# Kernel optimization log

Measured on AMD Instinct MI355X. Metric: run time of the kernel, lower is better.

The kernel has to match this reference:

```python
import jax, jax.numpy as jnp
import numpy as np

B, N_PER, F_IN, HID, DEG = 64, 1024, 64, 128, 16
N = B * N_PER
E = N * DEG

def _ceil_k(k):
    return -((-4 * k) // 5)  # ceil(0.8 * k), static python int

def setup_inputs():
    key = jax.random.key(0)
    ks = jax.random.split(key, 16)
    x = jax.random.normal(ks[0], (N, F_IN), jnp.float32)
    # edges are intra-graph: local endpoints in [0, N_PER) offset by graph id
    loc = jax.random.randint(ks[1], (2, E), 0, N_PER, jnp.int32)
    gid = jnp.repeat(jnp.arange(B, dtype=jnp.int32), E // B)
    edge_index = loc + gid[None, :] * N_PER
    batch = jnp.repeat(jnp.arange(B, dtype=jnp.int32), N_PER)
    def lin(k, fi, fo):
        s = 1.0 / float(np.sqrt(fi))
        return jax.random.uniform(k, (fi, fo), jnp.float32, -s, s)
    inp = dict(x=x, edge_index=edge_index, batch=batch)
    inp["Wr1"] = lin(ks[2], F_IN, HID); inp["Wn1"] = lin(ks[3], F_IN, HID); inp["b1"] = jnp.zeros((HID,), jnp.float32)
    inp["Wr2"] = lin(ks[4], HID, HID); inp["Wn2"] = lin(ks[5], HID, HID); inp["b2"] = jnp.zeros((HID,), jnp.float32)
    inp["Wr3"] = lin(ks[6], HID, HID); inp["Wn3"] = lin(ks[7], HID, HID); inp["b3"] = jnp.zeros((HID,), jnp.float32)
    inp["p1"] = jax.random.normal(ks[8], (HID,), jnp.float32)
    inp["p2"] = jax.random.normal(ks[9], (HID,), jnp.float32)
    inp["p3"] = jax.random.normal(ks[10], (HID,), jnp.float32)
    inp["l1w"] = lin(ks[11], 2 * HID, HID); inp["l1b"] = jnp.zeros((HID,), jnp.float32)
    inp["l2w"] = lin(ks[12], HID, 2); inp["l2b"] = jnp.zeros((2,), jnp.float32)
    return inp

def _graph_conv(x, src, dst, emask, Wr, Wn, b, n_nodes):
    # x'_i = W1 x_i + sum_{j->i} W2 x_j + b ; masked edges contribute 0
    msg = x[src] * emask[:, None]                                  # [E, H]
    agg = jax.ops.segment_sum(msg, dst, num_segments=n_nodes)     # [N, H]
    return x @ Wr + agg @ Wn + b

def _topk_pool(x, src, dst, emask, p, k_prev):
    # PyG TopKPooling: score = x.p/||p||, keep ceil(0.8*n) per graph,
    # x_out = x[perm] * tanh(score[perm]); relabel+filter edges
    k_new = _ceil_k(k_prev)
    s = (x @ p) / jnp.linalg.norm(p)                               # [B*k_prev]
    vals, idx = jax.lax.top_k(s.reshape(B, k_prev), k_new)        # [B, k_new]
    perm = (idx + jnp.arange(B, dtype=idx.dtype)[:, None] * k_prev).reshape(-1)
    x_new = x[perm] * jnp.tanh(vals.reshape(-1))[:, None]
    inv = jnp.full((B * k_prev,), -1, jnp.int32).at[perm].set(jnp.arange(B * k_new, dtype=jnp.int32))
    ns, nd = inv[src], inv[dst]
    valid = emask * ((ns >= 0) & (nd >= 0)).astype(x.dtype)
    return x_new, jnp.maximum(ns, 0), jnp.maximum(nd, 0), valid, k_new

def _readout(x, k):
    b = jnp.repeat(jnp.arange(B, dtype=jnp.int32), k)
    gmax = jax.ops.segment_max(x, b, num_segments=B)
    gmean = jax.ops.segment_sum(x, b, num_segments=B) / k
    return jnp.concatenate([gmax, gmean], axis=1)                  # [B, 2H]

def reference(x, edge_index, batch, Wr1, Wn1, b1, Wr2, Wn2, b2, Wr3, Wn3, b3, p1, p2, p3, l1w, l1b, l2w, l2b):
    src, dst = edge_index[0], edge_index[1]
    emask = jnp.ones((E,), x.dtype)
    k = N_PER
    convs = [(Wr1, Wn1, b1), (Wr2, Wn2, b2), (Wr3, Wn3, b3)]
    pools = [p1, p2, p3]
    xs = []
    for (Wr, Wn, bb), p in zip(convs, pools):
        x = jax.nn.relu(_graph_conv(x, src, dst, emask, Wr, Wn, bb, B * k))
        x, src, dst, emask, k = _topk_pool(x, src, dst, emask, p, k)
        xs.append(_readout(x, k))
    h = xs[0] + xs[1] + xs[2]
    h = jax.nn.relu(h @ l1w + l1b)
    # F.dropout(p=0.5) skipped: eval-mode reference
    h = jax.nn.relu(h @ l2w + l2b)
    return jax.nn.log_softmax(h, axis=-1)
```

## Files before the change

### kernel.cpp

```cpp
#include <hip/hip_runtime.h>
#include <hip/hip_bf16.h>
#include <math.h>

#define NN   65536
#define NPER 1024
#define NE   1048576
#define NB   64

typedef __attribute__((ext_vector_type(8))) short short8;
typedef __attribute__((ext_vector_type(4))) float f32x4;


__global__ __launch_bounds__(256) void count_kernel(const int* __restrict__ ei, int* __restrict__ cnt){
  int e = blockIdx.x*256 + threadIdx.x;
  if (e < NE) atomicAdd(&cnt[ei[NE + e]], 1);
}

__global__ __launch_bounds__(1024) void scan1_kernel(const int* __restrict__ cnt,
      int* __restrict__ loc, int* __restrict__ bsum){
  __shared__ int wsum[16];
  int t = threadIdx.x;
  int i = blockIdx.x*1024 + t;
  int lane = t & 63, wid = t >> 6;
  int v = cnt[i];
  int s = v;
  #pragma unroll
  for (int d = 1; d < 64; d <<= 1){
    int src = (lane >= d) ? (lane - d) : lane;
    int u = __shfl(s, src);
    if (lane >= d) s += u;
  }
  if (lane == 63) wsum[wid] = s;
  __syncthreads();
  if (wid == 0){
    int ws = (lane < 16) ? wsum[lane] : 0;
    #pragma unroll
    for (int d = 1; d < 16; d <<= 1){
      int src = (lane >= d) ? (lane - d) : lane;
      int u = __shfl(ws, src);
      if (lane >= d) ws += u;
    }
    if (lane < 16) wsum[lane] = ws;
  }
  __syncthreads();
  int base = (wid > 0) ? wsum[wid - 1] : 0;
  loc[i] = base + s - v;
  if (t == 1023) bsum[blockIdx.x] = base + s;
}

__global__ __launch_bounds__(64) void scan2_kernel(const int* __restrict__ bsum, int* __restrict__ boff){
  int t = threadIdx.x;
  int v = bsum[t];
  int s = v;
  #pragma unroll
  for (int d = 1; d < 64; d <<= 1){
    int src = (t >= d) ? (t - d) : t;
    int u = __shfl(s, src);
    if (t >= d) s += u;
  }
  boff[t] = s - v;
}

__global__ __launch_bounds__(1024) void scan3_kernel(const int* __restrict__ loc, const int* __restrict__ boff,
      int* __restrict__ off, int* __restrict__ cursor){
  int i = blockIdx.x*1024 + threadIdx.x;
  int v = loc[i] + boff[blockIdx.x];
  off[i] = v;
  cursor[i] = v;
  if (i == NN - 1) off[NN] = NE;
}

__global__ __launch_bounds__(256) void fill_kernel(const int* __restrict__ ei, int* cursor, int* __restrict__ adj){
  int e = blockIdx.x*256 + threadIdx.x;
  if (e < NE){
    int pos = atomicAdd(&cursor[ei[NE + e]], 1);
    adj[pos] = ei[e];
  }
}


__global__ __launch_bounds__(1024) void compact_kernel(const int* __restrict__ off, const int* __restrict__ adj,
      const float* __restrict__ scale, const int* __restrict__ alive,
      int* __restrict__ adj2, float* __restrict__ scl2, int* __restrict__ deg2){
  int w = blockIdx.x*16 + ((int)threadIdx.x >> 6);
  int lane = threadIdx.x & 63;
  if (!alive[w]){ if (lane == 0) deg2[w] = 0; return; }
  int s0 = off[w], s1 = off[w+1];
  int base = s0;
  for (int e0 = s0; e0 < s1; e0 += 64){
    int e = e0 + lane;
    bool okE = e < s1;
    int s = adj[okE ? e : (s1 - 1)];
    float t = scale[s];
    bool keep = okE && (t != 0.f);
    unsigned long long m = __ballot(keep);
    int pos = base + __popcll(m & ((1ull << lane) - 1ull));
    if (keep){ adj2[pos] = s << 9; scl2[pos] = t; }
    base += __popcll(m);
  }
  if (lane == 0) deg2[w] = base - s0;
}


__global__ __launch_bounds__(1024) void gather_kernel(const float* __restrict__ x, int F,
      const int* __restrict__ off, const int* __restrict__ adjB, const float* __restrict__ scl,
      const int* __restrict__ deg2, float* __restrict__ agg, const int* __restrict__ alive){
  int bid = blockIdx.x;
  bid = (bid & 7) * (gridDim.x >> 3) + (bid >> 3);
  int w = bid*16 + ((int)threadIdx.x >> 6);
  int lane = threadIdx.x & 63;
  if (alive && !alive[w]) return;
  int s0 = off[w];
  int s1 = deg2 ? (s0 + deg2[w]) : off[w+1];
  if (F == 64){
    const char* xb = (const char*)x + (lane & 15)*16;
    int sub = lane >> 4;
    float4 a0 = make_float4(0.f,0.f,0.f,0.f), a1 = a0;
    if (s1 > s0){
      for (int e = s0; e < s1; e += 8){
        int e0 = e + sub, e1 = e + 4 + sub;
        bool ok0 = e0 < s1, ok1 = e1 < s1;
        size_t oA = (size_t)(unsigned)adjB[ok0 ? e0 : (s1 - 1)] << 8;
        size_t oB = (size_t)(unsigned)adjB[ok1 ? e1 : (s1 - 1)] << 8;
        float t0 = ok0 ? 1.f : 0.f, t1 = ok1 ? 1.f : 0.f;
        float4 vA = *(const float4*)(xb + oA);
        float4 vB = *(const float4*)(xb + oB);
        a0.x = fmaf(vA.x, t0, a0.x); a0.y = fmaf(vA.y, t0, a0.y);
        a0.z = fmaf(vA.z, t0, a0.z); a0.w = fmaf(vA.w, t0, a0.w);
        a1.x = fmaf(vB.x, t1, a1.x); a1.y = fmaf(vB.y, t1, a1.y);
        a1.z = fmaf(vB.z, t1, a1.z); a1.w = fmaf(vB.w, t1, a1.w);
      }
    }
    a0.x += a1.x; a0.y += a1.y; a0.z += a1.z; a0.w += a1.w;
    #pragma unroll
    for (int m = 16; m <= 32; m <<= 1){
      a0.x += __shfl_xor(a0.x, m);
      a0.y += __shfl_xor(a0.y, m);
      a0.z += __shfl_xor(a0.z, m);
      a0.w += __shfl_xor(a0.w, m);
    }
    if (lane < 16) *(float4*)&agg[(size_t)w*128 + (lane & 15)*4] = a0;
  } else {
    const char* xb = (const char*)x + (lane & 31)*16;
    int sub = lane >> 5;
    float4 a[4];
    #pragma unroll
    for (int i = 0; i < 4; ++i) a[i] = make_float4(0.f,0.f,0.f,0.f);
    if (s1 > s0){
      for (int e = s0; e < s1; e += 8){
        int ss[4]; float tv[4];
        #pragma unroll
        for (int i = 0; i < 4; ++i){
          int ei = e + 2*i + sub;
          bool okE = ei < s1;
          int ii = okE ? ei : (s1 - 1);
          ss[i] = adjB[ii];
          tv[i] = okE ? scl[ii] : 0.f;
        }
        #pragma unroll
        for (int i = 0; i < 4; ++i){
          float4 v = *(const float4*)(xb + (size_t)(unsigned)ss[i]);
          a[i].x = fmaf(v.x, tv[i], a[i].x);
          a[i].y = fmaf(v.y, tv[i], a[i].y);
          a[i].z = fmaf(v.z, tv[i], a[i].z);
          a[i].w = fmaf(v.w, tv[i], a[i].w);
        }
      }
    }
    float4 r;
    r.x = (a[0].x + a[1].x) + (a[2].x + a[3].x);
    r.y = (a[0].y + a[1].y) + (a[2].y + a[3].y);
    r.z = (a[0].z + a[1].z) + (a[2].z + a[3].z);
    r.w = (a[0].w + a[1].w) + (a[2].w + a[3].w);
    r.x += __shfl_xor(r.x, 32);
    r.y += __shfl_xor(r.y, 32);
    r.z += __shfl_xor(r.z, 32);
    r.w += __shfl_xor(r.w, 32);
    if (lane < 32) *(float4*)&agg[(size_t)w*128 + (lane & 31)*4] = r;
  }
}


__global__ __launch_bounds__(256) void wsplit_all_kernel(
      const float* __restrict__ Wr0, const float* __restrict__ Wn0,
      const float* __restrict__ Wr1, const float* __restrict__ Wn1,
      const float* __restrict__ Wr2, const float* __restrict__ Wn2,
      unsigned short* __restrict__ WTh, unsigned short* __restrict__ WTl){
  int idx = blockIdx.x*256 + threadIdx.x;
  int rel, Kcat, Kx, base;
  const float *Wr, *Wn;
  if (idx < 16384){ rel = idx;          Kcat = 128; Kx = 64;  base = 0;     Wr = Wr0; Wn = Wn0; }
  else if (idx < 49152){ rel = idx - 16384; Kcat = 256; Kx = 128; base = 16384; Wr = Wr1; Wn = Wn1; }
  else { rel = idx - 49152; Kcat = 256; Kx = 128; base = 49152; Wr = Wr2; Wn = Wn2; }
  int c = rel & 127, k = rel >> 7;
  float w = (k < Kx) ? Wr[k*128 + c] : Wn[(k - Kx)*128 + c];
  __hip_bfloat16 h = __float2bfloat16(w);
  float hf = __bfloat162float(h);
  __hip_bfloat16 l = __float2bfloat16(w - hf);
  WTh[base + c*Kcat + k] = reinterpret_cast<unsigned short&>(h);
  WTl[base + c*Kcat + k] = reinterpret_cast<unsigned short&>(l);
}


__global__ __launch_bounds__(256, 2) void conv_kernel(const float* __restrict__ xsrc, int strideX, int ntx,
      const float* aggb, int nta,
      const unsigned short* __restrict__ WTh, const unsigned short* __restrict__ WTl, int Kcat,
      const float* __restrict__ bias, const float* __restrict__ p, const float* __restrict__ scaleX,
      float* yout, float* __restrict__ score){
  __shared__ unsigned short XhL[128*32], XlL[128*32];
  __shared__ unsigned short WhL[128*32], WlL[128*32];
  __shared__ float sbuf[128*2];
  const int tid = threadIdx.x;
  const int row0 = blockIdx.x * 128;
  const int srow = tid & 127;
  const int shalf = tid >> 7;
  const int lane = tid & 63;
  const int wid = tid >> 6;
  const int wr = wid >> 1, wc = wid & 1;
  const int l15 = lane & 15, lkq = lane >> 4;

  const float xscale = scaleX ? scaleX[row0 + srow] : 1.f;

  f32x4 acc[4][4];
  #pragma unroll
  for (int m = 0; m < 4; ++m)
    #pragma unroll
    for (int j = 0; j < 4; ++j)
      acc[m][j] = (f32x4){0.f, 0.f, 0.f, 0.f};

  const int nt = ntx + nta;
  for (int t = 0; t < nt; ++t){
    __syncthreads();
    {
      const float* Xs   = (t < ntx) ? xsrc : aggb;
      const int stride  = (t < ntx) ? strideX : 128;
      const int kc      = (t < ntx) ? t*32 : (t - ntx)*32;
      const float sc    = (t < ntx) ? xscale : 1.f;
      #pragma unroll
      for (int kq2 = 0; kq2 < 2; ++kq2){
        const int kq = shalf*2 + kq2;
        const float* xp = Xs + (size_t)(row0 + srow)*stride + kc + kq*8;
        float4 v0 = *(const float4*)(xp);
        float4 v1 = *(const float4*)(xp + 4);
        float vv[8] = {v0.x*sc, v0.y*sc, v0.z*sc, v0.w*sc,
                       v1.x*sc, v1.y*sc, v1.z*sc, v1.w*sc};
        short8 hs, ls;
        #pragma unroll
        for (int q = 0; q < 8; ++q){
          __hip_bfloat16 h = __float2bfloat16(vv[q]);
          float hf = __bfloat162float(h);
          __hip_bfloat16 lo = __float2bfloat16(vv[q] - hf);
          hs[q] = reinterpret_cast<short&>(h);
          ls[q] = reinterpret_cast<short&>(lo);
        }
        const int kqph = kq ^ (srow & 3);
        *(short8*)&XhL[srow*32 + kqph*8] = hs;
        *(short8*)&XlL[srow*32 + kqph*8] = ls;
      }
      const int kcw = t*32;
      #pragma unroll
      for (int kq2 = 0; kq2 < 2; ++kq2){
        const int kq = shalf*2 + kq2;
        short8 h = *(const short8*)&WTh[(size_t)srow*Kcat + kcw + kq*8];
        short8 l = *(const short8*)&WTl[(size_t)srow*Kcat + kcw + kq*8];
        const int kqph = kq ^ (srow & 3);
        *(short8*)&WhL[srow*32 + kqph*8] = h;
        *(short8*)&WlL[srow*32 + kqph*8] = l;
      }
    }
    __syncthreads();
    short8 bh[4], bl[4];
    #pragma unroll
    for (int j = 0; j < 4; ++j){
      const int col = wc*64 + j*16 + l15;
      const int offb = col*32 + (lkq ^ (col & 3))*8;
      bh[j] = *(const short8*)&WhL[offb];
      bl[j] = *(const short8*)&WlL[offb];
    }
    #pragma unroll
    for (int m = 0; m < 4; ++m){
      const int row = wr*64 + m*16 + l15;
      const int offa = row*32 + (lkq ^ (row & 3))*8;
      short8 ah = *(const short8*)&XhL[offa];
      short8 al = *(const short8*)&XlL[offa];
      #pragma unroll
      for (int j = 0; j < 4; ++j){
        acc[m][j] = __builtin_amdgcn_mfma_f32_16x16x32_bf16(ah, bh[j], acc[m][j], 0, 0, 0);
        acc[m][j] = __builtin_amdgcn_mfma_f32_16x16x32_bf16(ah, bl[j], acc[m][j], 0, 0, 0);
        acc[m][j] = __builtin_amdgcn_mfma_f32_16x16x32_bf16(al, bh[j], acc[m][j], 0, 0, 0);
      }
    }
  }

  #pragma unroll
  for (int m = 0; m < 4; ++m){
    float prt[4] = {0.f, 0.f, 0.f, 0.f};
    #pragma unroll
    for (int j = 0; j < 4; ++j){
      const int col = wc*64 + j*16 + l15;
      const float bcol = bias[col];
      const float pcol = p[col];
      f32x4 a = acc[m][j];
      #pragma unroll
      for (int r = 0; r < 4; ++r){
        const int row = wr*64 + m*16 + lkq*4 + r;
        float y = fmaxf(a[r] + bcol, 0.f);
        yout[(size_t)(row0 + row)*128 + col] = y;
        prt[r] = fmaf(y, pcol, prt[r]);
      }
    }
    #pragma unroll
    for (int r = 0; r < 4; ++r){
      #pragma unroll
      for (int msk = 8; msk >= 1; msk >>= 1) prt[r] += __shfl_xor(prt[r], msk);
      if (l15 == 0) sbuf[(wr*64 + m*16 + lkq*4 + r)*2 + wc] = prt[r];
    }
  }
  __syncthreads();
  if (tid < 128) score[row0 + tid] = sbuf[tid*2] + sbuf[tid*2 + 1];
}


__global__ __launch_bounds__(1024) void topk_kernel(const float* __restrict__ score, const int* __restrict__ alive_cur,
      int* __restrict__ alive_next, float* __restrict__ scale, const float* __restrict__ p, int m){
  __shared__ float lv[1024];
  __shared__ int   li[1024];
  __shared__ float rnorm;
  const int g = blockIdx.x, t = threadIdx.x;
  if (t < 64){
    float v0 = p[t], v1 = p[t + 64];
    float ss = v0*v0 + v1*v1;
    #pragma unroll
    for (int mm = 32; mm >= 1; mm >>= 1) ss += __shfl_xor(ss, mm);
    if (t == 0) rnorm = rsqrtf(ss);
  }
  const int node = g*NPER + t;
  bool ok = alive_cur ? (alive_cur[node] != 0) : true;
  float v = ok ? score[node] : -INFINITY;
  int idx = node;
  alive_next[node] = 0;
  scale[node] = 0.f;

  auto cex_shfl = [&](int stride, bool dirUp){
    float vj = __shfl_xor(v, stride);
    int   ij = __shfl_xor(idx, stride);
    bool iAmLow = (t & stride) == 0;
    bool mineFirst = (v > vj) || (v == vj && idx < ij);
    bool takeMine = ((dirUp == iAmLow) == mineFirst);
    v   = takeMine ? v   : vj;
    idx = takeMine ? idx : ij;
  };
  auto cex_lds = [&](int stride, bool dirUp){
    __syncthreads();
    lv[t] = v; li[t] = idx;
    __syncthreads();
    float vj = lv[t ^ stride];
    int   ij = li[t ^ stride];
    bool iAmLow = (t & stride) == 0;
    bool mineFirst = (v > vj) || (v == vj && idx < ij);
    bool takeMine = ((dirUp == iAmLow) == mineFirst);
    v   = takeMine ? v   : vj;
    idx = takeMine ? idx : ij;
  };

  #pragma unroll
  for (int size = 2; size <= 64; size <<= 1){
    const bool dirUp = (t & size) == 0;
    for (int stride = size >> 1; stride >= 1; stride >>= 1)
      cex_shfl(stride, dirUp);
  }
  #pragma unroll
  for (int size = 128; size <= 1024; size <<= 1){
    const bool dirUp = (t & size) == 0;
    for (int stride = size >> 1; stride >= 64; stride >>= 1)
      cex_lds(stride, dirUp);
    for (int stride = 32; stride >= 1; stride >>= 1)
      cex_shfl(stride, dirUp);
  }

  if (t < m){
    alive_next[idx] = 1;
    scale[idx] = tanhf(v * rnorm);
  }
}


__global__ __launch_bounds__(1024) void readout_kernel(const float* __restrict__ y,
      const int* __restrict__ alive, const float* __restrict__ scale,
      float* __restrict__ h, int m){
  __shared__ float smx[64][17];
  __shared__ float ssm[64][17];
  int g = blockIdx.x;
  int fq = blockIdx.y;
  int t = threadIdx.x;
  int c  = t >> 4;
  int lf = t & 15;
  int f  = fq*16 + lf;
  int base = g*NPER;
  float mx[4] = {-INFINITY, -INFINITY, -INFINITY, -INFINITY};
  float sm[4] = {0.f, 0.f, 0.f, 0.f};
  #pragma unroll
  for (int i = 0; i < 16; i += 4){
    #pragma unroll
    for (int q = 0; q < 4; ++q){
      int node = base + c + (i + q)*64;
      int al = alive[node];
      float o = y[(size_t)node*128 + f] * scale[node];
      mx[q] = al ? fmaxf(mx[q], o) : mx[q];
      sm[q] += o;
    }
  }
  float mxa = fmaxf(fmaxf(mx[0], mx[1]), fmaxf(mx[2], mx[3]));
  float sma = (sm[0] + sm[1]) + (sm[2] + sm[3]);
  smx[c][lf] = mxa; ssm[c][lf] = sma;
  __syncthreads();
  for (int s = 32; s > 0; s >>= 1){
    if (c < s){
      smx[c][lf] = fmaxf(smx[c][lf], smx[c+s][lf]);
      ssm[c][lf] += ssm[c+s][lf];
    }
    __syncthreads();
  }
  if (c == 0){
    h[g*256 + f]       += smx[0][lf];
    h[g*256 + 128 + f] += ssm[0][lf] / (float)m;
  }
}


__global__ __launch_bounds__(128) void final_kernel(const float* __restrict__ h,
      const float* __restrict__ l1w, const float* __restrict__ l1b,
      const float* __restrict__ l2w, const float* __restrict__ l2b,
      float* __restrict__ out){
  int g = blockIdx.x, t = threadIdx.x;
  __shared__ float hrow[256];
  __shared__ float red0[128], red1[128];
  hrow[t]       = h[g*256 + t];
  hrow[t + 128] = h[g*256 + 128 + t];
  __syncthreads();
  float a = l1b[t];
  for (int k = 0; k < 256; ++k) a = fmaf(hrow[k], l1w[k*128 + t], a);
  a = fmaxf(a, 0.f);
  red0[t] = a * l2w[t*2 + 0];
  red1[t] = a * l2w[t*2 + 1];
  __syncthreads();
  for (int s = 64; s > 0; s >>= 1){
    if (t < s){ red0[t] += red0[t + s]; red1[t] += red1[t + s]; }
    __syncthreads();
  }
  if (t == 0){
    float z0 = fmaxf(red0[0] + l2b[0], 0.f);
    float z1 = fmaxf(red1[0] + l2b[1], 0.f);
    float mz = fmaxf(z0, z1);
    float lse = mz + logf(expf(z0 - mz) + expf(z1 - mz));
    out[g*2 + 0] = z0 - lse;
    out[g*2 + 1] = z1 - lse;
  }
}


static inline size_t alignup(size_t x){ return (x + 255) & ~(size_t)255; }

extern "C" void kernel_launch(void* const* d_in, const int* in_sizes, int n_in,
                              void* d_out, int out_size, void* d_ws, size_t ws_size,
                              hipStream_t stream) {
  const float* x_in = (const float*)d_in[0];
  const int*   ei   = (const int*)d_in[1];
  const float* Wr[3] = {(const float*)d_in[3], (const float*)d_in[6], (const float*)d_in[9]};
  const float* Wn[3] = {(const float*)d_in[4], (const float*)d_in[7], (const float*)d_in[10]};
  const float* bs[3] = {(const float*)d_in[5], (const float*)d_in[8], (const float*)d_in[11]};
  const float* ps[3] = {(const float*)d_in[12], (const float*)d_in[13], (const float*)d_in[14]};
  const float* l1w = (const float*)d_in[15];
  const float* l1b = (const float*)d_in[16];
  const float* l2w = (const float*)d_in[17];
  const float* l2b = (const float*)d_in[18];
  float* out = (float*)d_out;

  char* w = (char*)d_ws;
  size_t o = 0;
  auto take = [&](size_t bytes) -> void* { void* p = w + o; o = alignup(o + bytes); return p; };
  int*   off    = (int*)  take((size_t)(NN + 1) * 4);
  int*   adj    = (int*)  take((size_t)NE * 4);
  int*   adj2   = (int*)  take((size_t)NE * 4);
  float* scl2   = (float*)take((size_t)NE * 4);
  int*   deg2   = (int*)  take((size_t)NN * 4);
  int*   cnt    = (int*)  take((size_t)NN * 4);
  int*   loc    = (int*)  take((size_t)NN * 4);
  int*   cursor = (int*)  take((size_t)NN * 4);
  int*   bsum   = (int*)  take(64 * 4);
  int*   boff   = (int*)  take(64 * 4);
  int*   aliveA = (int*)  take((size_t)NN * 4);
  int*   aliveB = (int*)  take((size_t)NN * 4);
  float* scale  = (float*)take((size_t)NN * 4);
  float* score  = (float*)take((size_t)NN * 4);
  float* h      = (float*)take((size_t)NB * 256 * 4);
  unsigned short* WTh = (unsigned short*)take((size_t)81920 * 2);
  unsigned short* WTl = (unsigned short*)take((size_t)81920 * 2);
  float* A      = (float*)take((size_t)NN * 128 * 4);
  float* Bb     = (float*)take((size_t)NN * 128 * 4);
  (void)ws_size; (void)n_in; (void)in_sizes; (void)out_size;

  hipMemsetAsync(cnt, 0, (size_t)NN * 4, stream);
  count_kernel<<<NE/256, 256, 0, stream>>>(ei, cnt);
  scan1_kernel<<<NN/1024, 1024, 0, stream>>>(cnt, loc, bsum);
  scan2_kernel<<<1, 64, 0, stream>>>(bsum, boff);
  scan3_kernel<<<NN/1024, 1024, 0, stream>>>(loc, boff, off, cursor);
  fill_kernel<<<NE/256, 256, 0, stream>>>(ei, cursor, adj);
  hipMemsetAsync(h, 0, (size_t)NB * 256 * 4, stream);
  wsplit_all_kernel<<<320, 256, 0, stream>>>(Wr[0], Wn[0], Wr[1], Wn[1], Wr[2], Wn[2], WTh, WTl);

  const int MS[3]   = {820, 656, 525};
  const int WOFF[3] = {0, 16384, 49152};
  const int KCAT[3] = {128, 256, 256};
  int* aliveCur = nullptr;
  int* aliveNext = aliveA;
  float* bufs[2] = {Bb, A};
  for (int l = 0; l < 3; ++l){
    const int Kx = (l == 0) ? 64 : 128;
    const int Ka = (l == 0) ? 64 : 128;
    float* aggb = bufs[l & 1];
    if (l == 0){
      gather_kernel<<<NN/16, 1024, 0, stream>>>(x_in, 64, off, adj, nullptr, nullptr, aggb, nullptr);
      conv_kernel<<<NN/128, 256, 0, stream>>>(x_in, 64, Kx/32, aggb, Ka/32, WTh + WOFF[0], WTl + WOFF[0], KCAT[0],
                                              bs[0], ps[0], nullptr, aggb, score);
    } else {
      const float* ysrc = bufs[(l - 1) & 1];
      compact_kernel<<<NN/16, 1024, 0, stream>>>(off, adj, scale, aliveCur, adj2, scl2, deg2);
      gather_kernel<<<NN/16, 1024, 0, stream>>>(ysrc, 128, off, adj2, scl2, deg2, aggb, aliveCur);
      conv_kernel<<<NN/128, 256, 0, stream>>>(ysrc, 128, Kx/32, aggb, Ka/32, WTh + WOFF[l], WTl + WOFF[l], KCAT[l],
                                              bs[l], ps[l], scale, aggb, score);
    }
    topk_kernel<<<NB, 1024, 0, stream>>>(score, aliveCur, aliveNext, scale, ps[l], MS[l]);
    readout_kernel<<<dim3(NB, 8), 1024, 0, stream>>>(aggb, aliveNext, scale, h, MS[l]);
    aliveCur = aliveNext;
    aliveNext = (l == 0) ? aliveB : aliveA;
  }
  final_kernel<<<NB, 128, 0, stream>>>(h, l1w, l1b, l2w, l2b, out);
}
```

Baseline: 325.8 us.

## Fuse CSR build per graph and merge topk, readout and compaction into one kernel

Builds the CSR in a single per-graph kernel that uses a shared-memory histogram, scan and fill. This replaces the count/scan/fill chain, its memsets and its global atomics, and it relies on edges being contiguous and intra-graph per block of EPG. It also merges topk, readout and edge compaction into one per-graph tail kernel that keeps scale and alive in shared memory, which removes several launches and global round trips. The cost is that the readout and compaction now run on only 64 blocks, one per graph, so parallelism drops sharply for those phases.

```diff
diff --git a/kernel.cpp b/kernel.cpp
--- a/kernel.cpp
+++ b/kernel.cpp
@@ -6,23 +6,31 @@
 #define NPER 1024
 #define NE   1048576
 #define NB   64
+#define EPG  16384
 
 typedef __attribute__((ext_vector_type(8))) short short8;
 typedef __attribute__((ext_vector_type(4))) float f32x4;
 
 
-__global__ __launch_bounds__(256) void count_kernel(const int* __restrict__ ei, int* __restrict__ cnt){
-  int e = blockIdx.x*256 + threadIdx.x;
-  if (e < NE) atomicAdd(&cnt[ei[NE + e]], 1);
-}
-
-__global__ __launch_bounds__(1024) void scan1_kernel(const int* __restrict__ cnt,
-      int* __restrict__ loc, int* __restrict__ bsum){
+__global__ __launch_bounds__(1024) void csr_kernel(const int* __restrict__ ei,
+      int* __restrict__ off, int* __restrict__ adj){
+  __shared__ int hist[1024];
   __shared__ int wsum[16];
-  int t = threadIdx.x;
-  int i = blockIdx.x*1024 + t;
+  const int g = blockIdx.x, t = threadIdx.x;
+  const int ebase = g*EPG, nbase = g*NPER;
+  hist[t] = 0;
+  __syncthreads();
+  int srcs[16], dls[16];
+  #pragma unroll
+  for (int i = 0; i < 16; ++i){
+    int e = ebase + t + i*1024;
+    srcs[i] = ei[e];
+    dls[i]  = ei[NE + e] - nbase;
+    atomicAdd(&hist[dls[i]], 1);
+  }
+  __syncthreads();
+  int v = hist[t];
   int lane = t & 63, wid = t >> 6;
-  int v = cnt[i];
   int s = v;
   #pragma unroll
   for (int d = 1; d < 64; d <<= 1){
@@ -44,61 +52,17 @@
   }
   __syncthreads();
   int base = (wid > 0) ? wsum[wid - 1] : 0;
-  loc[i] = base + s - v;
-  if (t == 1023) bsum[blockIdx.x] = base + s;
-}
-
-__global__ __launch_bounds__(64) void scan2_kernel(const int* __restrict__ bsum, int* __restrict__ boff){
-  int t = threadIdx.x;
-  int v = bsum[t];
-  int s = v;
-  #pragma unroll
-  for (int d = 1; d < 64; d <<= 1){
-    int src = (t >= d) ? (t - d) : t;
-    int u = __shfl(s, src);
-    if (t >= d) s += u;
-  }
-  boff[t] = s - v;
-}
-
-__global__ __launch_bounds__(1024) void scan3_kernel(const int* __restrict__ loc, const int* __restrict__ boff,
-      int* __restrict__ off, int* __restrict__ cursor){
-  int i = blockIdx.x*1024 + threadIdx.x;
-  int v = loc[i] + boff[blockIdx.x];
-  off[i] = v;
-  cursor[i] = v;
-  if (i == NN - 1) off[NN] = NE;
-}
-
-__global__ __launch_bounds__(256) void fill_kernel(const int* __restrict__ ei, int* cursor, int* __restrict__ adj){
-  int e = blockIdx.x*256 + threadIdx.x;
-  if (e < NE){
-    int pos = atomicAdd(&cursor[ei[NE + e]], 1);
-    adj[pos] = ei[e];
-  }
-}
-
-
-__global__ __launch_bounds__(1024) void compact_kernel(const int* __restrict__ off, const int* __restrict__ adj,
-      const float* __restrict__ scale, const int* __restrict__ alive,
-      int* __restrict__ adj2, float* __restrict__ scl2, int* __restrict__ deg2){
-  int w = blockIdx.x*16 + ((int)threadIdx.x >> 6);
-  int lane = threadIdx.x & 63;
-  if (!alive[w]){ if (lane == 0) deg2[w] = 0; return; }
-  int s0 = off[w], s1 = off[w+1];
-  int base = s0;
-  for (int e0 = s0; e0 < s1; e0 += 64){
-    int e = e0 + lane;
-    bool okE = e < s1;
-    int s = adj[okE ? e : (s1 - 1)];
-    float t = scale[s];
-    bool keep = okE && (t != 0.f);
-    unsigned long long m = __ballot(keep);
-    int pos = base + __popcll(m & ((1ull << lane) - 1ull));
-    if (keep){ adj2[pos] = s << 9; scl2[pos] = t; }
-    base += __popcll(m);
-  }
-  if (lane == 0) deg2[w] = base - s0;
+  int excl = base + s - v;
+  __syncthreads();
+  hist[t] = excl;
+  off[nbase + t] = ebase + excl;
+  if (g == NB - 1 && t == 1023) off[NN] = NE;
+  __syncthreads();
+  #pragma unroll
+  for (int i = 0; i < 16; ++i){
+    int pos = atomicAdd(&hist[dls[i]], 1);
+    adj[ebase + pos] = srcs[i];
+  }
 }
 
 
@@ -321,10 +285,18 @@
 }
 
 
-__global__ __launch_bounds__(1024) void topk_kernel(const float* __restrict__ score, const int* __restrict__ alive_cur,
-      int* __restrict__ alive_next, float* __restrict__ scale, const float* __restrict__ p, int m){
+__global__ __launch_bounds__(1024) void tail_kernel(const float* __restrict__ score,
+      const int* __restrict__ alive_cur, int* __restrict__ alive_next,
+      float* __restrict__ scale, const float* __restrict__ p, int m,
+      const float* __restrict__ y, float* __restrict__ h, int firstLevel,
+      const int* __restrict__ off, const int* __restrict__ adj,
+      int* __restrict__ adj2, float* __restrict__ scl2, int* __restrict__ deg2, int doCompact){
   __shared__ float lv[1024];
   __shared__ int   li[1024];
+  __shared__ float sscale[1024];
+  __shared__ int   salive[1024];
+  __shared__ float smx[8*128];
+  __shared__ float ssm[8*128];
   __shared__ float rnorm;
   const int g = blockIdx.x, t = threadIdx.x;
   if (t < 64){
@@ -334,12 +306,15 @@
     for (int mm = 32; mm >= 1; mm >>= 1) ss += __shfl_xor(ss, mm);
     if (t == 0) rnorm = rsqrtf(ss);
   }
+  sscale[t] = 0.f;
+  salive[t] = 0;
   const int node = g*NPER + t;
   bool ok = alive_cur ? (alive_cur[node] != 0) : true;
   float v = ok ? score[node] : -INFINITY;
   int idx = node;
   alive_next[node] = 0;
   scale[node] = 0.f;
+  __syncthreads();
 
   auto cex_shfl = [&](int stride, bool dirUp){
     float vj = __shfl_xor(v, stride);
@@ -379,51 +354,75 @@
   }
 
   if (t < m){
+    float tv = tanhf(v * rnorm);
     alive_next[idx] = 1;
-    scale[idx] = tanhf(v * rnorm);
-  }
-}
-
-
-__global__ __launch_bounds__(1024) void readout_kernel(const float* __restrict__ y,
-      const int* __restrict__ alive, const float* __restrict__ scale,
-      float* __restrict__ h, int m){
-  __shared__ float smx[64][17];
-  __shared__ float ssm[64][17];
-  int g = blockIdx.x;
-  int fq = blockIdx.y;
-  int t = threadIdx.x;
-  int c  = t >> 4;
-  int lf = t & 15;
-  int f  = fq*16 + lf;
-  int base = g*NPER;
-  float mx[4] = {-INFINITY, -INFINITY, -INFINITY, -INFINITY};
-  float sm[4] = {0.f, 0.f, 0.f, 0.f};
-  #pragma unroll
-  for (int i = 0; i < 16; i += 4){
-    #pragma unroll
-    for (int q = 0; q < 4; ++q){
-      int node = base + c + (i + q)*64;
-      int al = alive[node];
-      float o = y[(size_t)node*128 + f] * scale[node];
-      mx[q] = al ? fmaxf(mx[q], o) : mx[q];
-      sm[q] += o;
-    }
-  }
-  float mxa = fmaxf(fmaxf(mx[0], mx[1]), fmaxf(mx[2], mx[3]));
-  float sma = (sm[0] + sm[1]) + (sm[2] + sm[3]);
-  smx[c][lf] = mxa; ssm[c][lf] = sma;
-  __syncthreads();
-  for (int s = 32; s > 0; s >>= 1){
-    if (c < s){
-      smx[c][lf] = fmaxf(smx[c][lf], smx[c+s][lf]);
-      ssm[c][lf] += ssm[c+s][lf];
-    }
+    scale[idx] = tv;
+    int loc = idx - g*NPER;
+    sscale[loc] = tv;
+    salive[loc] = 1;
+  }
+  __syncthreads();
+
+  {
+    const int f = t & 127, grp = t >> 7;
+    const int nb0 = grp*128;
+    const float* yg = y + (size_t)(g*NPER)*128 + f;
+    float mx[4] = {-INFINITY, -INFINITY, -INFINITY, -INFINITY};
+    float sm[4] = {0.f, 0.f, 0.f, 0.f};
+    #pragma unroll 4
+    for (int i = 0; i < 128; i += 4){
+      #pragma unroll
+      for (int q = 0; q < 4; ++q){
+        int nl = nb0 + i + q;
+        float o = yg[(size_t)nl*128] * sscale[nl];
+        mx[q] = salive[nl] ? fmaxf(mx[q], o) : mx[q];
+        sm[q] += o;
+      }
+    }
+    float mxa = fmaxf(fmaxf(mx[0], mx[1]), fmaxf(mx[2], mx[3]));
+    float sma = (sm[0] + sm[1]) + (sm[2] + sm[3]);
+    smx[grp*128 + f] = mxa; ssm[grp*128 + f] = sma;
     __syncthreads();
-  }
-  if (c == 0){
-    h[g*256 + f]       += smx[0][lf];
-    h[g*256 + 128 + f] += ssm[0][lf] / (float)m;
+    #pragma unroll
+    for (int s2 = 4; s2 >= 1; s2 >>= 1){
+      if (grp < s2){
+        smx[grp*128 + f] = fmaxf(smx[grp*128 + f], smx[(grp+s2)*128 + f]);
+        ssm[grp*128 + f] += ssm[(grp+s2)*128 + f];
+      }
+      __syncthreads();
+    }
+    if (grp == 0){
+      if (firstLevel){
+        h[g*256 + f]       = smx[f];
+        h[g*256 + 128 + f] = ssm[f] / (float)m;
+      } else {
+        h[g*256 + f]       += smx[f];
+        h[g*256 + 128 + f] += ssm[f] / (float)m;
+      }
+    }
+  }
+
+  if (doCompact){
+    const int lane2 = t & 63, wv = t >> 6;
+    for (int n2 = 0; n2 < 64; ++n2){
+      int wl = wv*64 + n2;
+      int w = g*NPER + wl;
+      if (!salive[wl]){ if (lane2 == 0) deg2[w] = 0; continue; }
+      int s0 = off[w], s1 = off[w+1];
+      int bse = s0;
+      for (int e0 = s0; e0 < s1; e0 += 64){
+        int e = e0 + lane2;
+        bool okE = e < s1;
+        int sN = adj[okE ? e : (s1 - 1)];
+        float tv = sscale[sN - g*NPER];
+        bool keep = okE && (tv != 0.f);
+        unsigned long long mmask = __ballot(keep);
+        int pos = bse + __popcll(mmask & ((1ull << lane2) - 1ull));
+        if (keep){ adj2[pos] = sN << 9; scl2[pos] = tv; }
+        bse += __popcll(mmask);
+      }
+      if (lane2 == 0) deg2[w] = bse - s0;
+    }
   }
 }
 
@@ -484,11 +483,6 @@
   int*   adj2   = (int*)  take((size_t)NE * 4);
   float* scl2   = (float*)take((size_t)NE * 4);
   int*   deg2   = (int*)  take((size_t)NN * 4);
-  int*   cnt    = (int*)  take((size_t)NN * 4);
-  int*   loc    = (int*)  take((size_t)NN * 4);
-  int*   cursor = (int*)  take((size_t)NN * 4);
-  int*   bsum   = (int*)  take(64 * 4);
-  int*   boff   = (int*)  take(64 * 4);
   int*   aliveA = (int*)  take((size_t)NN * 4);
   int*   aliveB = (int*)  take((size_t)NN * 4);
   float* scale  = (float*)take((size_t)NN * 4);
@@ -500,13 +494,7 @@
   float* Bb     = (float*)take((size_t)NN * 128 * 4);
   (void)ws_size; (void)n_in; (void)in_sizes; (void)out_size;
 
-  hipMemsetAsync(cnt, 0, (size_t)NN * 4, stream);
-  count_kernel<<<NE/256, 256, 0, stream>>>(ei, cnt);
-  scan1_kernel<<<NN/1024, 1024, 0, stream>>>(cnt, loc, bsum);
-  scan2_kernel<<<1, 64, 0, stream>>>(bsum, boff);
-  scan3_kernel<<<NN/1024, 1024, 0, stream>>>(loc, boff, off, cursor);
-  fill_kernel<<<NE/256, 256, 0, stream>>>(ei, cursor, adj);
-  hipMemsetAsync(h, 0, (size_t)NB * 256 * 4, stream);
+  csr_kernel<<<NB, 1024, 0, stream>>>(ei, off, adj);
   wsplit_all_kernel<<<320, 256, 0, stream>>>(Wr[0], Wn[0], Wr[1], Wn[1], Wr[2], Wn[2], WTh, WTl);
 
   const int MS[3]   = {820, 656, 525};
@@ -525,13 +513,13 @@
                                               bs[0], ps[0], nullptr, aggb, score);
     } else {
       const float* ysrc = bufs[(l - 1) & 1];
-      compact_kernel<<<NN/16, 1024, 0, stream>>>(off, adj, scale, aliveCur, adj2, scl2, deg2);
       gather_kernel<<<NN/16, 1024, 0, stream>>>(ysrc, 128, off, adj2, scl2, deg2, aggb, aliveCur);
       conv_kernel<<<NN/128, 256, 0, stream>>>(ysrc, 128, Kx/32, aggb, Ka/32, WTh + WOFF[l], WTl + WOFF[l], KCAT[l],
                                               bs[l], ps[l], scale, aggb, score);
     }
-    topk_kernel<<<NB, 1024, 0, stream>>>(score, aliveCur, aliveNext, scale, ps[l], MS[l]);
-    readout_kernel<<<dim3(NB, 8), 1024, 0, stream>>>(aggb, aliveNext, scale, h, MS[l]);
+    tail_kernel<<<NB, 1024, 0, stream>>>(score, aliveCur, aliveNext, scale, ps[l], MS[l],
+                                         aggb, h, (l == 0) ? 1 : 0,
+                                         off, adj, adj2, scl2, deg2, (l < 2) ? 1 : 0);
     aliveCur = aliveNext;
     aliveNext = (l == 0) ? aliveB : aliveA;
   }
```

Measured after the change: 316.5 us. 2.9% less time.
